# Kernel tuning notes

Hardware: AMD Instinct MI355X
Metric: run time of the kernel (lower is better)

Reference implementation:

```python
import jax, jax.numpy as jnp
import numpy as np
import math

B_SZ, L_SEQ, IN_DIM, D_MODEL, OUT_DIM = 8, 4096, 256, 512, 256
RMIN, RMAX = 0.8, 0.99


def setup_inputs() -> dict:
    key = jax.random.key(0)
    ks = jax.random.split(key, 9)
    inputs = jax.random.normal(ks[0], (B_SZ, L_SEQ, IN_DIM), dtype=jnp.float32)
    # A-parameterization per LRUBlock.init_A
    u1 = jax.random.uniform(ks[1], (D_MODEL,), dtype=jnp.float32)
    u2 = jax.random.uniform(ks[2], (D_MODEL,), dtype=jnp.float32)
    nu_log = jnp.log(-0.5 * jnp.log(u1 * (RMAX + RMIN) * (RMAX - RMIN) + RMIN ** 2))
    theta_log = jnp.log(2 * math.pi * u2)
    # NB: original stores gamma (not log gamma) and exponentiates it in forward; replicate.
    gamma_log = jnp.sqrt(1.0 - jnp.exp(-jnp.exp(nu_log)) ** 2)
    B_re = jax.random.uniform(ks[3], (D_MODEL, IN_DIM), dtype=jnp.float32) / math.sqrt(2 * IN_DIM)
    B_im = jax.random.uniform(ks[4], (D_MODEL, IN_DIM), dtype=jnp.float32) / math.sqrt(2 * IN_DIM)
    C_re = jax.random.uniform(ks[5], (OUT_DIM, D_MODEL), dtype=jnp.float32) / math.sqrt(D_MODEL)
    C_im = jax.random.uniform(ks[6], (OUT_DIM, D_MODEL), dtype=jnp.float32) / math.sqrt(D_MODEL)
    D = jax.random.uniform(ks[7], (OUT_DIM, IN_DIM), dtype=jnp.float32) / math.sqrt(IN_DIM)
    return {"inputs": inputs, "nu_log": nu_log, "theta_log": theta_log,
            "gamma_log": gamma_log, "B_re": B_re, "B_im": B_im,
            "C_re": C_re, "C_im": C_im, "D": D}


def reference(inputs, nu_log, theta_log, gamma_log, B_re, B_im, C_re, C_im, D):
    # skip connection: [b, l, in] x [out, in] -> [b, l, out]
    skip = jnp.einsum('blh,dh->bld', inputs, D)
    L = inputs.shape[1]
    # diagonal complex transition A = exp(-exp(nu) + i*exp(theta)), [d_model]
    A = jnp.exp(jax.lax.complex(-jnp.exp(nu_log), jnp.exp(theta_log)))
    Bc = jax.lax.complex(B_re, B_im) * jnp.exp(gamma_log)[:, None]
    # input projection u = inputs @ B^T : [b, l, d_model] complex64
    u = jnp.einsum('blh,dh->bld', inputs.astype(jnp.complex64), Bc)
    # convolution kernel H[d, t] = A[d]^t, linear conv via length-2L FFT
    H = A[:, None] ** jnp.arange(L)  # [d_model, L]
    n = 2 * L
    h_f = jnp.fft.fft(H, n=n, axis=1)          # [d_model, 2L]
    u_f = jnp.fft.fft(u, n=n, axis=1)          # [b, 2L, d_model]
    x = jnp.fft.ifft(u_f * h_f.T, axis=1)[:, :L]  # [b, L, d_model] complex64
    y = jnp.einsum('blh,nh->bln', x, jax.lax.complex(C_re, C_im)).real + skip
    return (x, y)
```

## Files before the change

### kernel.cpp

```cpp
#include <hip/hip_runtime.h>
#include <hip/hip_bf16.h>
#include <math.h>

#define B_SZ 8
#define L_SEQ 4096
#define IN_DIM 256
#define D_MODEL 512
#define OUT_DIM 256
#define M_ROWS (B_SZ*L_SEQ)
#define CH 64
#define NCH (L_SEQ/CH)

#define Y_OFF ((size_t)M_ROWS*D_MODEL)

#define XIM_B   ((size_t)0)
#define WT_B    ((size_t)33554432)
#define CDT_B   ((size_t)34078720)
#define S_B     ((size_t)34734080)

typedef __attribute__((ext_vector_type(8))) short short8;
typedef __attribute__((ext_vector_type(4))) float f32x4;
typedef unsigned short ushort_t;

__device__ __forceinline__ unsigned short f2b(float f) {
    unsigned u = __float_as_uint(f);
    unsigned r = u + 0x7FFF + ((u >> 16) & 1);
    return (unsigned short)(r >> 16);
}
__device__ __forceinline__ float b2f(unsigned v) {
    return __uint_as_float(v << 16);
}
__device__ __forceinline__ unsigned pk2(float lo, float hi) {
    __hip_bfloat162 h = __float22bfloat162_rn(make_float2(lo, hi));
    return *(unsigned*)&h;
}

__global__ void build_wt(const float* __restrict__ B_re, const float* __restrict__ B_im,
                         const float* __restrict__ gamma_log, ushort_t* __restrict__ Wt) {
    int idx = blockIdx.x*256 + threadIdx.x;
    int r = idx >> 8, h = idx & 255;
    int d = r >> 1, comp = r & 1;
    float eg = expf(gamma_log[d]);
    float v = (comp ? B_im[d*256 + h] : B_re[d*256 + h]) * eg;
    Wt[idx] = f2b(v);
}

__global__ void build_cdt(const float* __restrict__ C_re, const float* __restrict__ C_im,
                          const float* __restrict__ Dm, ushort_t* __restrict__ CDt) {
    int idx = blockIdx.x*256 + threadIdx.x;
    int n = idx / 1280, k = idx % 1280;
    float v;
    if      (k < 512)  v =  C_re[n*512 + k];
    else if (k < 1024) v = -C_im[n*512 + (k-512)];
    else               v =  Dm[n*256 + (k-1024)];
    CDt[idx] = f2b(v);
}

__global__ __launch_bounds__(256) void gemm_u(const float* __restrict__ inp, const ushort_t* __restrict__ Wt,
                                              ushort_t* __restrict__ xpair) {
    __shared__ ushort_t Al[128][40];
    __shared__ ushort_t Bl[128][40];
    const int tid = threadIdx.x;
    const int nwg = gridDim.x * gridDim.y;
    int orig = blockIdx.y * gridDim.x + blockIdx.x;
    int wg = (orig & 7) * (nwg >> 3) + (orig >> 3);
    const int row0 = (wg / gridDim.x) * 128, col0 = (wg % gridDim.x) * 128;
    const int wave = tid >> 6, lane = tid & 63;
    const int wr = wave >> 1, wc = wave & 1;
    const int fr = lane & 15, kg = lane >> 4;
    const int sr = tid >> 1, sh = (tid & 1)*16;
    f32x4 acc[4][4] = {};
    for (int k0 = 0; k0 < IN_DIM; k0 += 32) {
        const float* ap = inp + (size_t)(row0+sr)*IN_DIM + k0 + sh;
        float4 a0 = *(const float4*)(ap+0), a1 = *(const float4*)(ap+4);
        float4 a2 = *(const float4*)(ap+8), a3 = *(const float4*)(ap+12);
        const ushort_t* bp = Wt + (size_t)(col0+sr)*IN_DIM + k0 + sh;
        uint4 b0 = *(const uint4*)bp, b1 = *(const uint4*)(bp+8);
        unsigned av[8];
        av[0]=pk2(a0.x,a0.y); av[1]=pk2(a0.z,a0.w);
        av[2]=pk2(a1.x,a1.y); av[3]=pk2(a1.z,a1.w);
        av[4]=pk2(a2.x,a2.y); av[5]=pk2(a2.z,a2.w);
        av[6]=pk2(a3.x,a3.y); av[7]=pk2(a3.z,a3.w);
        __syncthreads();
        *(uint4*)&Al[sr][sh]   = *(uint4*)&av[0];
        *(uint4*)&Al[sr][sh+8] = *(uint4*)&av[4];
        *(uint4*)&Bl[sr][sh]   = b0;
        *(uint4*)&Bl[sr][sh+8] = b1;
        __syncthreads();
        short8 af[4], bf[4];
        #pragma unroll
        for (int m = 0; m < 4; ++m) af[m] = *(const short8*)&Al[wr*64 + m*16 + fr][kg*8];
        #pragma unroll
        for (int n = 0; n < 4; ++n) bf[n] = *(const short8*)&Bl[wc*64 + n*16 + fr][kg*8];
        #pragma unroll
        for (int m = 0; m < 4; ++m)
            #pragma unroll
            for (int n = 0; n < 4; ++n)
                acc[m][n] = __builtin_amdgcn_mfma_f32_16x16x32_bf16(af[m], bf[n], acc[m][n], 0, 0, 0);
    }
    #pragma unroll
    for (int m = 0; m < 4; ++m)
        #pragma unroll
        for (int n = 0; n < 4; ++n) {
            int col = col0 + wc*64 + n*16 + fr;
            #pragma unroll
            for (int j = 0; j < 4; ++j) {
                int row = row0 + wr*64 + m*16 + kg*4 + j;
                xpair[(size_t)row*1024 + col] = f2b(acc[m][n][j]);
            }
        }
}

__global__ __launch_bounds__(256) void gemm_y(const float* __restrict__ xre, const ushort_t* __restrict__ xim,
                                              const float* __restrict__ inp, const ushort_t* __restrict__ CDt,
                                              float* __restrict__ y) {
    __shared__ ushort_t Al[128][40];
    __shared__ ushort_t Bl[128][40];
    const int tid = threadIdx.x;
    const int nwg = gridDim.x * gridDim.y;
    int orig = blockIdx.y * gridDim.x + blockIdx.x;
    int wg = (orig & 7) * (nwg >> 3) + (orig >> 3);
    const int row0 = (wg / gridDim.x) * 128, col0 = (wg % gridDim.x) * 128;
    const int wave = tid >> 6, lane = tid & 63;
    const int wr = wave >> 1, wc = wave & 1;
    const int fr = lane & 15, kg = lane >> 4;
    const int sr = tid >> 1, sh = (tid & 1)*16;
    f32x4 acc[4][4] = {};
    for (int k0 = 0; k0 < 1280; k0 += 32) {
        unsigned av[8];
        if (k0 < 512) {
            const float* ap = xre + (size_t)(row0+sr)*D_MODEL + k0 + sh;
            #pragma unroll
            for (int i = 0; i < 4; ++i) {
                float4 f = *(const float4*)(ap + i*4);
                av[2*i]   = pk2(f.x, f.y);
                av[2*i+1] = pk2(f.z, f.w);
            }
        } else if (k0 < 1024) {
            const ushort_t* ap = xim + (size_t)(row0+sr)*D_MODEL + (k0-512) + sh;
            *(uint4*)&av[0] = *(const uint4*)ap;
            *(uint4*)&av[4] = *(const uint4*)(ap+8);
        } else {
            const float* ap = inp + (size_t)(row0+sr)*IN_DIM + (k0-1024) + sh;
            #pragma unroll
            for (int i = 0; i < 4; ++i) {
                float4 f = *(const float4*)(ap + i*4);
                av[2*i]   = pk2(f.x, f.y);
                av[2*i+1] = pk2(f.z, f.w);
            }
        }
        const ushort_t* bp = CDt + (size_t)(col0+sr)*1280 + k0 + sh;
        uint4 b0 = *(const uint4*)bp, b1 = *(const uint4*)(bp+8);
        __syncthreads();
        *(uint4*)&Al[sr][sh]   = *(uint4*)&av[0];
        *(uint4*)&Al[sr][sh+8] = *(uint4*)&av[4];
        *(uint4*)&Bl[sr][sh]   = b0;
        *(uint4*)&Bl[sr][sh+8] = b1;
        __syncthreads();
        short8 af[4], bf[4];
        #pragma unroll
        for (int m = 0; m < 4; ++m) af[m] = *(const short8*)&Al[wr*64 + m*16 + fr][kg*8];
        #pragma unroll
        for (int n = 0; n < 4; ++n) bf[n] = *(const short8*)&Bl[wc*64 + n*16 + fr][kg*8];
        #pragma unroll
        for (int m = 0; m < 4; ++m)
            #pragma unroll
            for (int n = 0; n < 4; ++n)
                acc[m][n] = __builtin_amdgcn_mfma_f32_16x16x32_bf16(af[m], bf[n], acc[m][n], 0, 0, 0);
    }
    #pragma unroll
    for (int m = 0; m < 4; ++m)
        #pragma unroll
        for (int n = 0; n < 4; ++n) {
            int col = col0 + wc*64 + n*16 + fr;
            #pragma unroll
            for (int j = 0; j < 4; ++j) {
                int row = row0 + wr*64 + m*16 + kg*4 + j;
                y[(size_t)row*OUT_DIM + col] = acc[m][n][j];
            }
        }
}

__global__ void scan_phase1(const unsigned* __restrict__ xp,
                            const float* __restrict__ nu_log, const float* __restrict__ theta_log,
                            float2* __restrict__ s) {
    int idx = blockIdx.x*256 + threadIdx.x;
    int d = idx & (D_MODEL-1);
    int c = (idx >> 9) & (NCH-1);
    int b = idx >> 15;
    float en = expf(nu_log[d]), et = expf(theta_log[d]);
    float mag = expf(-en);
    float ar = mag*cosf(et), ai = mag*sinf(et);
    float hr = 0.f, hi = 0.f;
    size_t off = ((size_t)(b*L_SEQ) + c*CH)*D_MODEL + d;
    #pragma unroll 4
    for (int j = 0; j < CH; ++j) {
        unsigned p = xp[off];
        float ur = b2f(p & 0xffffu), ui = b2f(p >> 16);
        float nr = ar*hr - ai*hi + ur;
        float ni = ar*hi + ai*hr + ui;
        hr = nr; hi = ni;
        off += D_MODEL;
    }
    s[idx] = make_float2(hr, hi);
}

__global__ void scan_phase2(const float* __restrict__ nu_log, const float* __restrict__ theta_log,
                            float2* __restrict__ s) {
    int idx = blockIdx.x*256 + threadIdx.x;
    int d = idx & (D_MODEL-1);
    int b = idx >> 9;
    float en = expf(nu_log[d]), et = expf(theta_log[d]);
    float mag = expf(-(float)CH*en);
    float ang = (float)CH*et;
    float aCr = mag*cosf(ang), aCi = mag*sinf(ang);
    float er = 0.f, ei = 0.f;
    float2* sp = s + (size_t)b*NCH*D_MODEL + d;
    for (int c8 = 0; c8 < NCH; c8 += 8) {
        float2 v[8];
        #pragma unroll
        for (int i = 0; i < 8; ++i) v[i] = sp[(size_t)(c8+i)*D_MODEL];
        #pragma unroll
        for (int i = 0; i < 8; ++i) {
            sp[(size_t)(c8+i)*D_MODEL] = make_float2(er, ei);
            float nr = aCr*er - aCi*ei + v[i].x;
            float ni = aCr*ei + aCi*er + v[i].y;
            er = nr; ei = ni;
        }
    }
}

__global__ void scan_phase3(unsigned* __restrict__ xp, ushort_t* __restrict__ xim,
                            const float* __restrict__ nu_log, const float* __restrict__ theta_log,
                            const float2* __restrict__ s) {
    int idx = blockIdx.x*256 + threadIdx.x;
    int d = idx & (D_MODEL-1);
    int c = (idx >> 9) & (NCH-1);
    int b = idx >> 15;
    float en = expf(nu_log[d]), et = expf(theta_log[d]);
    float mag = expf(-en);
    float ar = mag*cosf(et), ai = mag*sinf(et);
    float2 carry = s[idx];
    float hr = carry.x, hi = carry.y;
    size_t off = ((size_t)(b*L_SEQ) + c*CH)*D_MODEL + d;
    #pragma unroll 4
    for (int j = 0; j < CH; ++j) {
        unsigned p = xp[off];
        float ur = b2f(p & 0xffffu), ui = b2f(p >> 16);
        float nr = ar*hr - ai*hi + ur;
        float ni = ar*hi + ai*hr + ui;
        hr = nr; hi = ni;
        xp[off] = __float_as_uint(hr);
        xim[off] = f2b(hi);
        off += D_MODEL;
    }
}

extern "C" void kernel_launch(void* const* d_in, const int* in_sizes, int n_in,
                              void* d_out, int out_size, void* d_ws, size_t ws_size,
                              hipStream_t stream) {
    const float* inp       = (const float*)d_in[0];
    const float* nu_log    = (const float*)d_in[1];
    const float* theta_log = (const float*)d_in[2];
    const float* gamma_log = (const float*)d_in[3];
    const float* B_re      = (const float*)d_in[4];
    const float* B_im      = (const float*)d_in[5];
    const float* C_re      = (const float*)d_in[6];
    const float* C_im      = (const float*)d_in[7];
    const float* Dm        = (const float*)d_in[8];
    float* out = (float*)d_out;
    char* wsb  = (char*)d_ws;
    ushort_t* Xim = (ushort_t*)(wsb + XIM_B);
    ushort_t* Wt  = (ushort_t*)(wsb + WT_B);
    ushort_t* CDt = (ushort_t*)(wsb + CDT_B);
    float2*   S   = (float2*)  (wsb + S_B);

    build_wt<<<1024, 256, 0, stream>>>(B_re, B_im, gamma_log, Wt);
    build_cdt<<<1280, 256, 0, stream>>>(C_re, C_im, Dm, CDt);

    dim3 gu(1024/128, M_ROWS/128);
    gemm_u<<<gu, 256, 0, stream>>>(inp, Wt, (ushort_t*)out);

    scan_phase1<<<(B_SZ*NCH*D_MODEL)/256, 256, 0, stream>>>((const unsigned*)out, nu_log, theta_log, S);
    scan_phase2<<<(B_SZ*D_MODEL)/256, 256, 0, stream>>>(nu_log, theta_log, S);
    scan_phase3<<<(B_SZ*NCH*D_MODEL)/256, 256, 0, stream>>>((unsigned*)out, Xim, nu_log, theta_log, S);

    dim3 gy(OUT_DIM/128, M_ROWS/128);
    gemm_y<<<gy, 256, 0, stream>>>(out, Xim, inp, CDt, out + Y_OFF);
}
```

Measured before the change: 267.7 us.

## Pre-convert input to bf16 and stage GEMM tiles via async global-to-LDS loads

Result: faster. 251.3 us (-6.1%).

```diff
diff --git a/kernel.cpp b/kernel.cpp
--- a/kernel.cpp
+++ b/kernel.cpp
@@ -14,13 +14,15 @@
 #define Y_OFF ((size_t)M_ROWS*D_MODEL)
 
 #define XIM_B   ((size_t)0)
-#define WT_B    ((size_t)33554432)
-#define CDT_B   ((size_t)34078720)
-#define S_B     ((size_t)34734080)
+#define INPB_B  ((size_t)33554432)
+#define WT_B    ((size_t)50331648)
+#define CDT_B   ((size_t)50855936)
+#define S_B     ((size_t)51511296)
 
 typedef __attribute__((ext_vector_type(8))) short short8;
 typedef __attribute__((ext_vector_type(4))) float f32x4;
 typedef unsigned short ushort_t;
+typedef unsigned int u32;
 
 __device__ __forceinline__ unsigned short f2b(float f) {
     unsigned u = __float_as_uint(f);
@@ -33,6 +35,18 @@
 __device__ __forceinline__ unsigned pk2(float lo, float hi) {
     __hip_bfloat162 h = __float22bfloat162_rn(make_float2(lo, hi));
     return *(unsigned*)&h;
+}
+__device__ __forceinline__ void async16(const void* g, void* l) {
+    __builtin_amdgcn_global_load_lds((const __attribute__((address_space(1))) u32*)g,
+                                     (__attribute__((address_space(3))) u32*)l, 16, 0, 0);
+}
+
+__global__ __launch_bounds__(256) void cvt_inp(const float* __restrict__ inp, ushort_t* __restrict__ inpb) {
+    size_t i = ((size_t)blockIdx.x*256 + threadIdx.x)*8;
+    float4 a = *(const float4*)(inp + i);
+    float4 b = *(const float4*)(inp + i + 4);
+    unsigned v[4] = { pk2(a.x,a.y), pk2(a.z,a.w), pk2(b.x,b.y), pk2(b.z,b.w) };
+    *(uint4*)(inpb + i) = *(uint4*)v;
 }
 
 __global__ void build_wt(const float* __restrict__ B_re, const float* __restrict__ B_im,
@@ -56,47 +70,45 @@
     CDt[idx] = f2b(v);
 }
 
-__global__ __launch_bounds__(256) void gemm_u(const float* __restrict__ inp, const ushort_t* __restrict__ Wt,
+__global__ __launch_bounds__(256) void gemm_u(const ushort_t* __restrict__ inpb, const ushort_t* __restrict__ Wt,
                                               ushort_t* __restrict__ xpair) {
-    __shared__ ushort_t Al[128][40];
-    __shared__ ushort_t Bl[128][40];
+    __shared__ ushort_t Al[128*64];
+    __shared__ ushort_t Bl[128*64];
     const int tid = threadIdx.x;
-    const int nwg = gridDim.x * gridDim.y;
-    int orig = blockIdx.y * gridDim.x + blockIdx.x;
-    int wg = (orig & 7) * (nwg >> 3) + (orig >> 3);
-    const int row0 = (wg / gridDim.x) * 128, col0 = (wg % gridDim.x) * 128;
+    int orig = blockIdx.x;
+    int wg = (orig & 7) * 256 + (orig >> 3);
+    const int row0 = (wg >> 3) * 128, col0 = (wg & 7) * 128;
     const int wave = tid >> 6, lane = tid & 63;
     const int wr = wave >> 1, wc = wave & 1;
     const int fr = lane & 15, kg = lane >> 4;
-    const int sr = tid >> 1, sh = (tid & 1)*16;
+    const int grow = tid >> 3, ggr = tid & 7;
     f32x4 acc[4][4] = {};
-    for (int k0 = 0; k0 < IN_DIM; k0 += 32) {
-        const float* ap = inp + (size_t)(row0+sr)*IN_DIM + k0 + sh;
-        float4 a0 = *(const float4*)(ap+0), a1 = *(const float4*)(ap+4);
-        float4 a2 = *(const float4*)(ap+8), a3 = *(const float4*)(ap+12);
-        const ushort_t* bp = Wt + (size_t)(col0+sr)*IN_DIM + k0 + sh;
-        uint4 b0 = *(const uint4*)bp, b1 = *(const uint4*)(bp+8);
-        unsigned av[8];
-        av[0]=pk2(a0.x,a0.y); av[1]=pk2(a0.z,a0.w);
-        av[2]=pk2(a1.x,a1.y); av[3]=pk2(a1.z,a1.w);
-        av[4]=pk2(a2.x,a2.y); av[5]=pk2(a2.z,a2.w);
-        av[6]=pk2(a3.x,a3.y); av[7]=pk2(a3.z,a3.w);
+    for (int k0 = 0; k0 < IN_DIM; k0 += 64) {
         __syncthreads();
-        *(uint4*)&Al[sr][sh]   = *(uint4*)&av[0];
-        *(uint4*)&Al[sr][sh+8] = *(uint4*)&av[4];
-        *(uint4*)&Bl[sr][sh]   = b0;
-        *(uint4*)&Bl[sr][sh+8] = b1;
+        #pragma unroll
+        for (int i = 0; i < 4; ++i) {
+            int row = grow + i*32;
+            async16(inpb + (size_t)(row0+row)*IN_DIM + k0 + ggr*8, &Al[(row*8 + ggr)*8]);
+        }
+        #pragma unroll
+        for (int i = 0; i < 4; ++i) {
+            int row = grow + i*32;
+            async16(Wt + (size_t)(col0+row)*IN_DIM + k0 + ggr*8, &Bl[(row*8 + ggr)*8]);
+        }
         __syncthreads();
-        short8 af[4], bf[4];
-        #pragma unroll
-        for (int m = 0; m < 4; ++m) af[m] = *(const short8*)&Al[wr*64 + m*16 + fr][kg*8];
-        #pragma unroll
-        for (int n = 0; n < 4; ++n) bf[n] = *(const short8*)&Bl[wc*64 + n*16 + fr][kg*8];
-        #pragma unroll
-        for (int m = 0; m < 4; ++m)
-            #pragma unroll
-            for (int n = 0; n < 4; ++n)
-                acc[m][n] = __builtin_amdgcn_mfma_f32_16x16x32_bf16(af[m], bf[n], acc[m][n], 0, 0, 0);
+        #pragma unroll
+        for (int kk = 0; kk < 2; ++kk) {
+            short8 af[4], bf[4];
+            #pragma unroll
+            for (int m = 0; m < 4; ++m) af[m] = *(const short8*)&Al[(wr*64 + m*16 + fr)*64 + kk*32 + kg*8];
+            #pragma unroll
+            for (int n = 0; n < 4; ++n) bf[n] = *(const short8*)&Bl[(wc*64 + n*16 + fr)*64 + kk*32 + kg*8];
+            #pragma unroll
+            for (int m = 0; m < 4; ++m)
+                #pragma unroll
+                for (int n = 0; n < 4; ++n)
+                    acc[m][n] = __builtin_amdgcn_mfma_f32_16x16x32_bf16(af[m], bf[n], acc[m][n], 0, 0, 0);
+        }
     }
     #pragma unroll
     for (int m = 0; m < 4; ++m)
@@ -112,61 +124,70 @@
 }
 
 __global__ __launch_bounds__(256) void gemm_y(const float* __restrict__ xre, const ushort_t* __restrict__ xim,
-                                              const float* __restrict__ inp, const ushort_t* __restrict__ CDt,
+                                              const ushort_t* __restrict__ inpb, const ushort_t* __restrict__ CDt,
                                               float* __restrict__ y) {
-    __shared__ ushort_t Al[128][40];
-    __shared__ ushort_t Bl[128][40];
+    __shared__ ushort_t Al[128*64];
+    __shared__ ushort_t Bl[128*64];
     const int tid = threadIdx.x;
-    const int nwg = gridDim.x * gridDim.y;
-    int orig = blockIdx.y * gridDim.x + blockIdx.x;
-    int wg = (orig & 7) * (nwg >> 3) + (orig >> 3);
-    const int row0 = (wg / gridDim.x) * 128, col0 = (wg % gridDim.x) * 128;
+    int orig = blockIdx.x;
+    int wg = (orig & 7) * 64 + (orig >> 3);
+    const int row0 = (wg >> 1) * 128, col0 = (wg & 1) * 128;
     const int wave = tid >> 6, lane = tid & 63;
     const int wr = wave >> 1, wc = wave & 1;
     const int fr = lane & 15, kg = lane >> 4;
-    const int sr = tid >> 1, sh = (tid & 1)*16;
+    const int grow = tid >> 3, ggr = tid & 7;
+    const int crow = tid >> 1, csh = (tid & 1)*32;
     f32x4 acc[4][4] = {};
-    for (int k0 = 0; k0 < 1280; k0 += 32) {
-        unsigned av[8];
-        if (k0 < 512) {
-            const float* ap = xre + (size_t)(row0+sr)*D_MODEL + k0 + sh;
+    for (int ks = 0; ks < 20; ++ks) {
+        const int k0 = ks*64;
+        __syncthreads();
+        if (ks < 8) {
+            const float* ap = xre + (size_t)(row0+crow)*D_MODEL + k0 + csh;
+            unsigned v[16];
+            #pragma unroll
+            for (int i = 0; i < 8; ++i) {
+                float4 f = *(const float4*)(ap + i*4);
+                v[2*i]   = pk2(f.x, f.y);
+                v[2*i+1] = pk2(f.z, f.w);
+            }
             #pragma unroll
             for (int i = 0; i < 4; ++i) {
-                float4 f = *(const float4*)(ap + i*4);
-                av[2*i]   = pk2(f.x, f.y);
-                av[2*i+1] = pk2(f.z, f.w);
-            }
-        } else if (k0 < 1024) {
-            const ushort_t* ap = xim + (size_t)(row0+sr)*D_MODEL + (k0-512) + sh;
-            *(uint4*)&av[0] = *(const uint4*)ap;
-            *(uint4*)&av[4] = *(const uint4*)(ap+8);
+                int row = grow + i*32;
+                async16(CDt + (size_t)(col0+row)*1280 + k0 + ggr*8, &Bl[(row*8 + ggr)*8]);
+            }
+            ushort_t* dst = &Al[crow*64 + csh];
+            #pragma unroll
+            for (int i = 0; i < 4; ++i) *(uint4*)(dst + i*8) = *(uint4*)&v[i*4];
         } else {
-            const float* ap = inp + (size_t)(row0+sr)*IN_DIM + (k0-1024) + sh;
+            const ushort_t* asrc;
+            size_t stride; int kc;
+            if (ks < 16) { asrc = xim;  stride = D_MODEL; kc = k0 - 512; }
+            else         { asrc = inpb; stride = IN_DIM;  kc = k0 - 1024; }
             #pragma unroll
             for (int i = 0; i < 4; ++i) {
-                float4 f = *(const float4*)(ap + i*4);
-                av[2*i]   = pk2(f.x, f.y);
-                av[2*i+1] = pk2(f.z, f.w);
-            }
-        }
-        const ushort_t* bp = CDt + (size_t)(col0+sr)*1280 + k0 + sh;
-        uint4 b0 = *(const uint4*)bp, b1 = *(const uint4*)(bp+8);
+                int row = grow + i*32;
+                async16(asrc + (size_t)(row0+row)*stride + kc + ggr*8, &Al[(row*8 + ggr)*8]);
+            }
+            #pragma unroll
+            for (int i = 0; i < 4; ++i) {
+                int row = grow + i*32;
+                async16(CDt + (size_t)(col0+row)*1280 + k0 + ggr*8, &Bl[(row*8 + ggr)*8]);
+            }
+        }
         __syncthreads();
-        *(uint4*)&Al[sr][sh]   = *(uint4*)&av[0];
-        *(uint4*)&Al[sr][sh+8] = *(uint4*)&av[4];
-        *(uint4*)&Bl[sr][sh]   = b0;
-        *(uint4*)&Bl[sr][sh+8] = b1;
-        __syncthreads();
-        short8 af[4], bf[4];
-        #pragma unroll
-        for (int m = 0; m < 4; ++m) af[m] = *(const short8*)&Al[wr*64 + m*16 + fr][kg*8];
-        #pragma unroll
-        for (int n = 0; n < 4; ++n) bf[n] = *(const short8*)&Bl[wc*64 + n*16 + fr][kg*8];
-        #pragma unroll
-        for (int m = 0; m < 4; ++m)
-            #pragma unroll
-            for (int n = 0; n < 4; ++n)
-                acc[m][n] = __builtin_amdgcn_mfma_f32_16x16x32_bf16(af[m], bf[n], acc[m][n], 0, 0, 0);
+        #pragma unroll
+        for (int kk = 0; kk < 2; ++kk) {
+            short8 af[4], bf[4];
+            #pragma unroll
+            for (int m = 0; m < 4; ++m) af[m] = *(const short8*)&Al[(wr*64 + m*16 + fr)*64 + kk*32 + kg*8];
+            #pragma unroll
+            for (int n = 0; n < 4; ++n) bf[n] = *(const short8*)&Bl[(wc*64 + n*16 + fr)*64 + kk*32 + kg*8];
+            #pragma unroll
+            for (int m = 0; m < 4; ++m)
+                #pragma unroll
+                for (int n = 0; n < 4; ++n)
+                    acc[m][n] = __builtin_amdgcn_mfma_f32_16x16x32_bf16(af[m], bf[n], acc[m][n], 0, 0, 0);
+        }
     }
     #pragma unroll
     for (int m = 0; m < 4; ++m)
@@ -270,21 +291,21 @@
     const float* Dm        = (const float*)d_in[8];
     float* out = (float*)d_out;
     char* wsb  = (char*)d_ws;
-    ushort_t* Xim = (ushort_t*)(wsb + XIM_B);
-    ushort_t* Wt  = (ushort_t*)(wsb + WT_B);
-    ushort_t* CDt = (ushort_t*)(wsb + CDT_B);
-    float2*   S   = (float2*)  (wsb + S_B);
+    ushort_t* Xim  = (ushort_t*)(wsb + XIM_B);
+    ushort_t* Inpb = (ushort_t*)(wsb + INPB_B);
+    ushort_t* Wt   = (ushort_t*)(wsb + WT_B);
+    ushort_t* CDt  = (ushort_t*)(wsb + CDT_B);
+    float2*   S    = (float2*)  (wsb + S_B);
 
     build_wt<<<1024, 256, 0, stream>>>(B_re, B_im, gamma_log, Wt);
     build_cdt<<<1280, 256, 0, stream>>>(C_re, C_im, Dm, CDt);
-
-    dim3 gu(1024/128, M_ROWS/128);
-    gemm_u<<<gu, 256, 0, stream>>>(inp, Wt, (ushort_t*)out);
+    cvt_inp<<<(M_ROWS*IN_DIM)/(256*8), 256, 0, stream>>>(inp, Inpb);
+
+    gemm_u<<<2048, 256, 0, stream>>>(Inpb, Wt, (ushort_t*)out);
 
     scan_phase1<<<(B_SZ*NCH*D_MODEL)/256, 256, 0, stream>>>((const unsigned*)out, nu_log, theta_log, S);
     scan_phase2<<<(B_SZ*D_MODEL)/256, 256, 0, stream>>>(nu_log, theta_log, S);
     scan_phase3<<<(B_SZ*NCH*D_MODEL)/256, 256, 0, stream>>>((unsigned*)out, Xim, nu_log, theta_log, S);
 
-    dim3 gy(OUT_DIM/128, M_ROWS/128);
-    gemm_y<<<gy, 256, 0, stream>>>(out, Xim, inp, CDt, out + Y_OFF);
-}
+    gemm_y<<<512, 256, 0, stream>>>(out, Xim, Inpb, CDt, out + Y_OFF);
+}
```
